# Optimization experiments

Measured on AMD Instinct MI355X. Metric: run time of the kernel, lower is better.

Reference implementation:

```python
import jax, jax.numpy as jnp
import numpy as np

B, H, W, D, C = 4, 16, 16, 16, 32

def setup_inputs() -> dict:
    key = jax.random.key(0)
    ks = jax.random.split(key, 13)
    s = 0.05
    return {
        "inputs": jax.random.normal(ks[0], (B, H, W, D, C), jnp.float32),
        "beta": jax.random.normal(ks[1], (1,), jnp.float32) * s,
        "wq": jax.random.normal(ks[2], (C, C), jnp.float32) * s,
        "bq": jax.random.normal(ks[3], (C,), jnp.float32) * s,
        "wk": jax.random.normal(ks[4], (C, C), jnp.float32) * s,
        "bk": jax.random.normal(ks[5], (C,), jnp.float32) * s,
        "wv": jax.random.normal(ks[6], (C, C), jnp.float32) * s,
        "bv": jax.random.normal(ks[7], (C,), jnp.float32) * s,
        "gamma": jax.random.normal(ks[8], (1,), jnp.float32) * s,
        "w_ch": jax.random.normal(ks[9], (1, 1, 4, C, C), jnp.float32) * s,
        "b_ch": jax.random.normal(ks[10], (C,), jnp.float32) * s,
        "w_pos": jax.random.normal(ks[11], (1, 1, 4, C, C), jnp.float32) * s,
        "b_pos": jax.random.normal(ks[12], (C,), jnp.float32) * s,
    }

def _conv3d_relu(x, w, b):
    # Conv3D kernel (1,1,4), VALID padding, then ReLU (activation='relu').
    y = jax.lax.conv_general_dilated(
        x, w, window_strides=(1, 1, 1), padding="VALID",
        dimension_numbers=("NDHWC", "DHWIO", "NDHWC"))
    return jax.nn.relu(y + b)

def reference(inputs, beta, wq, bq, wk, bk, wv, bv, gamma, w_ch, b_ch, w_pos, b_pos):
    b_, h, w, d, c = inputs.shape
    n = h * w * d  # flattened spatial-spectral volume

    # ---- Channel_attention (actually NxN spatial self-attention) ----
    q = inputs.reshape(b_, n, c)                       # (B,N,C)
    energy = jnp.einsum("bnc,bmc->bnm", q, q)          # (B,N,N) Q @ Q^T
    attn = jax.nn.softmax(energy, axis=-1)
    ca = jnp.einsum("bnm,bmc->bnc", attn, q)           # (B,N,C)
    ca = beta * ca.reshape(b_, h, w, d, c) + inputs

    # ---- Position_attention (CxC channel self-attention via 1x1x1 convs) ----
    Q = (jnp.einsum("bhwdc,cf->bhwdf", inputs, wq) + bq).reshape(b_, n, c)
    K = (jnp.einsum("bhwdc,cf->bhwdf", inputs, wk) + bk).reshape(b_, n, c)
    V = (jnp.einsum("bhwdc,cf->bhwdf", inputs, wv) + bv).reshape(b_, n, c)
    energy2 = jnp.einsum("bnc,bnf->bcf", Q, K)         # (B,C,C) = Q^T K
    attn2 = jax.nn.softmax(energy2, axis=-1)
    # out[b,n,f] = sum_c V[b,n,c] * attn2[b,f,c]  (V @ attn2^T per batch)
    pa = jnp.einsum("bnc,bfc->bnf", V, attn2)          # (B,N,C)
    pa = gamma * pa.reshape(b_, h, w, d, c) + inputs

    # ---- Attention_Embedding: conv3d(1,1,4)+relu on each branch, add ----
    # Dropout is identity at inference (training=False).
    out = _conv3d_relu(ca, w_ch, b_ch) + _conv3d_relu(pa, w_pos, b_pos)
    return out
```

## Files before the change

### kernel.cpp

```cpp
#include <hip/hip_runtime.h>
#include <cstddef>


typedef float f32x4 __attribute__((ext_vector_type(4)));
typedef short s16x8 __attribute__((ext_vector_type(8)));

#define SQRT_LOG2E 1.2011224087864498f
#define C2SHIFT    57.70780163555854f

__device__ inline unsigned cvtpk(float a, float b) {
  unsigned r;
  asm("v_cvt_pk_bf16_f32 %0, %1, %2" : "=v"(r) : "v"(a), "v"(b));
  return r;
}

__global__ __launch_bounds__(256) void k_prepgram(
    const float* __restrict__ x, ushort* __restrict__ xb, ushort* __restrict__ xtf,
    float* __restrict__ pG, float* __restrict__ pS)
{
  int bx = blockIdx.x, tid = threadIdx.x;
  if (bx < 256) {
    int t = bx * 256 + tid;
    const float4* xs = (const float4*)x;
    float4 v0 = xs[2 * t], v1 = xs[2 * t + 1];
    uint4 o;
    o.x = cvtpk(v0.x * SQRT_LOG2E, v0.y * SQRT_LOG2E);
    o.y = cvtpk(v0.z * SQRT_LOG2E, v0.w * SQRT_LOG2E);
    o.z = cvtpk(v1.x * SQRT_LOG2E, v1.y * SQRT_LOG2E);
    o.w = cvtpk(v1.z * SQRT_LOG2E, v1.w * SQRT_LOG2E);
    ((uint4*)xb)[t] = o;

    int b = t >> 14, r2 = t & 16383;
    int ktile = r2 >> 7, r3 = r2 & 127;
    int h = r3 >> 6, lane = r3 & 63;
    int g = lane >> 4, c = h * 16 + (lane & 15);
    const float* src = x + (((size_t)b * 4096 + ktile * 32 + 8 * g) * 32 + c);
    float w[8];
#pragma unroll
    for (int j = 0; j < 8; ++j) w[j] = src[(size_t)j * 32];
    uint4 u;
    u.x = cvtpk(w[0], w[1]); u.y = cvtpk(w[2], w[3]);
    u.z = cvtpk(w[4], w[5]); u.w = cvtpk(w[6], w[7]);
    ((uint4*)xtf)[(size_t)((b * 128 + ktile) * 2 + h) * 64 + lane] = u;
    return;
  }

  int gb = bx - 256;
  int b = gb >> 3, ks = gb & 7;
  int wid = tid >> 6, lane = tid & 63;
  int g = lane >> 4, c16 = lane & 15;
  f32x4 z = {0.f, 0.f, 0.f, 0.f};
  f32x4 G00 = z, G01 = z, G10 = z, G11 = z, s0 = z, s1 = z;
  s16x8 ones;
#pragma unroll
  for (int j = 0; j < 8; ++j) ones[j] = (short)0x3F80;
  int t0 = ks * 16 + wid * 4;
  for (int t = t0; t < t0 + 4; ++t) {
    s16x8 fr0, fr1;
    {
      const float* src = x + (((size_t)b * 4096 + t * 32 + 8 * g) * 32 + c16);
      float w[8];
#pragma unroll
      for (int j = 0; j < 8; ++j) w[j] = src[(size_t)j * 32];
      uint4 u2 = make_uint4(cvtpk(w[0], w[1]), cvtpk(w[2], w[3]),
                            cvtpk(w[4], w[5]), cvtpk(w[6], w[7]));
      fr0 = __builtin_bit_cast(s16x8, u2);
    }
    {
      const float* src = x + (((size_t)b * 4096 + t * 32 + 8 * g) * 32 + 16 + c16);
      float w[8];
#pragma unroll
      for (int j = 0; j < 8; ++j) w[j] = src[(size_t)j * 32];
      uint4 u2 = make_uint4(cvtpk(w[0], w[1]), cvtpk(w[2], w[3]),
                            cvtpk(w[4], w[5]), cvtpk(w[6], w[7]));
      fr1 = __builtin_bit_cast(s16x8, u2);
    }
    G00 = __builtin_amdgcn_mfma_f32_16x16x32_bf16(fr0, fr0, G00, 0, 0, 0);
    G01 = __builtin_amdgcn_mfma_f32_16x16x32_bf16(fr0, fr1, G01, 0, 0, 0);
    G10 = __builtin_amdgcn_mfma_f32_16x16x32_bf16(fr1, fr0, G10, 0, 0, 0);
    G11 = __builtin_amdgcn_mfma_f32_16x16x32_bf16(fr1, fr1, G11, 0, 0, 0);
    s0  = __builtin_amdgcn_mfma_f32_16x16x32_bf16(fr0, ones, s0, 0, 0, 0);
    s1  = __builtin_amdgcn_mfma_f32_16x16x32_bf16(fr1, ones, s1, 0, 0, 0);
  }
  int p = gb * 4 + wid;
  float* pg = pG + (size_t)p * 1024;
#pragma unroll
  for (int hr = 0; hr < 2; ++hr)
#pragma unroll
    for (int hc = 0; hc < 2; ++hc) {
      f32x4 v = hr ? (hc ? G11 : G10) : (hc ? G01 : G00);
#pragma unroll
      for (int r = 0; r < 4; ++r)
        pg[(16 * hr + 4 * g + r) * 32 + 16 * hc + c16] = v[r];
    }
  if (c16 == 0) {
#pragma unroll
    for (int hr = 0; hr < 2; ++hr) {
      f32x4 v = hr ? s1 : s0;
#pragma unroll
      for (int r = 0; r < 4; ++r) pS[p * 32 + 16 * hr + 4 * g + r] = v[r];
    }
  }
}

__global__ __launch_bounds__(1024) void k_alg(
    const float* __restrict__ pG, const float* __restrict__ pS,
    const float* __restrict__ wq, const float* __restrict__ bq,
    const float* __restrict__ wk, const float* __restrict__ bk,
    const float* __restrict__ wv, const float* __restrict__ bv,
    const float* __restrict__ gamma,
    const float* __restrict__ wpos, const float* __restrict__ bpos,
    float* __restrict__ w2, float* __restrict__ b2)
{
  __shared__ float G[1024], s[32], t1[1024], att[1024], M[1024], mvec[32];
  __shared__ float wqS[1024], wkS[1024], wvS[1024], wpoS[4096];
  int b = blockIdx.x, tid = threadIdx.x;
  if (tid < 256)      ((float4*)wqS)[tid] = ((const float4*)wq)[tid];
  else if (tid < 512) ((float4*)wkS)[tid - 256] = ((const float4*)wk)[tid - 256];
  else if (tid < 768) ((float4*)wvS)[tid - 512] = ((const float4*)wv)[tid - 512];
  ((float4*)wpoS)[tid] = ((const float4*)wpos)[tid];

  {
    const float* pg = pG + (size_t)b * 32 * 1024 + tid;
    float g0 = 0.f;
#pragma unroll
    for (int j = 0; j < 32; ++j) g0 += pg[(size_t)j * 1024];
    G[tid] = g0;
  }
  if (tid < 32) {
    const float* ps = pS + b * 32 * 32 + tid;
    float sv = 0.f;
#pragma unroll
    for (int j = 0; j < 32; ++j) sv += ps[j * 32];
    s[tid] = sv;
  }
  __syncthreads();

  int c = tid >> 5, f = tid & 31;
  float t = 0.f;
#pragma unroll
  for (int j = 0; j < 32; ++j) t = fmaf(G[c * 32 + j], wkS[j * 32 + f], t);
  t1[tid] = t;
  __syncthreads();
  float swk = 0.f, swq = 0.f;
#pragma unroll
  for (int j = 0; j < 32; ++j) {
    swk = fmaf(s[j], wkS[j * 32 + f], swk);
    swq = fmaf(s[j], wqS[j * 32 + c], swq);
  }
  float e = 0.f;
#pragma unroll
  for (int i = 0; i < 32; ++i) e = fmaf(wqS[i * 32 + c], t1[i * 32 + f], e);
  e += bq[c] * (swk + 4096.f * bk[f]) + swq * bk[f];
  float m_ = e;
  for (int off = 16; off; off >>= 1) m_ = fmaxf(m_, __shfl_xor(m_, off, 32));
  float pr = __expf(e - m_);
  float sum = pr;
  for (int off = 16; off; off >>= 1) sum += __shfl_xor(sum, off, 32);
  att[tid] = pr / sum;
  __syncthreads();
  float mm = 0.f;
#pragma unroll
  for (int j = 0; j < 32; ++j) mm = fmaf(wvS[c * 32 + j], att[f * 32 + j], mm);
  M[c * 32 + f] = mm;
  if (c == 0) {
    float mv = 0.f;
#pragma unroll
    for (int j = 0; j < 32; ++j) mv = fmaf(bv[j], att[f * 32 + j], mv);
    mvec[f] = mv;
  }
  __syncthreads();
  float gam = gamma[0];
  for (int kd = 0; kd < 4; ++kd) {
    float acc = 0.f;
#pragma unroll
    for (int j = 0; j < 32; ++j)
      acc = fmaf(M[c * 32 + j], wpoS[(kd * 32 + j) * 32 + f], acc);
    w2[((b * 4 + kd) * 32 + c) * 32 + f] = gam * acc + wpoS[(kd * 32 + c) * 32 + f];
  }
  if (c == 0) {
    float acc = 0.f;
#pragma unroll
    for (int kd = 0; kd < 4; ++kd)
#pragma unroll
      for (int j = 0; j < 32; ++j)
        acc = fmaf(mvec[j], wpoS[(kd * 32 + j) * 32 + tid], acc);
    b2[b * 32 + tid] = gam * acc + bpos[tid];
  }
}

union BigSh {
  char stage[4][2][8192];
  struct { f32x4 pO0[3][4][64]; f32x4 pO1[3][4][64]; float pL[3][4][64]; } ph1;
  struct { float4 wc[1024]; float4 wp[1024]; } ph2;
};

__global__ __launch_bounds__(1024) void k_fused(
    const ushort* __restrict__ xb, const ushort* __restrict__ xtf,
    const float* __restrict__ x, const float* __restrict__ beta,
    const float* __restrict__ wch, const float* __restrict__ bch,
    const float* __restrict__ w2, const float* __restrict__ b2,
    float* __restrict__ out)
{
  __shared__ BigSh u;
  __shared__ float sS[64][32];
  __shared__ float bcS[32], bpS[32];
  int rg = blockIdx.x, b = blockIdx.y, tid = threadIdx.x;
  if (tid < 32) { bcS[tid] = bch[tid]; bpS[tid] = b2[b * 32 + tid]; }

  int wid = tid >> 6, lane = tid & 63, g = lane >> 4, c16 = lane & 15;
  int wid2 = wid & 3, kh = wid >> 2;
  int qw = rg * 64 + wid2 * 16;
  const ushort* xbb = xb + ((size_t)b << 17);
  const ushort* xtb = xtf + (size_t)b * 131072;

  s16x8 qA = *(const s16x8*)(xbb + (qw + c16) * 32 + 8 * g);
  f32x4 z = {0.f, 0.f, 0.f, 0.f};
  f32x4 minit = {-C2SHIFT, -C2SHIFT, -C2SHIFT, -C2SHIFT};
  f32x4 oA0 = z, oA1 = z, lac = z;
  s16x8 ones;
#pragma unroll
  for (int j = 0; j < 8; ++j) ones[j] = (short)0x3F80;
  int kap = ((c16 >> 2) << 3) + (c16 & 3);
  int k0 = kh * 1024;

  int wtid = wid2 * 64 + lane;
  int srow = wtid >> 2, sslot = wtid & 3;
  int wslot = (sslot ^ (srow & 3)) << 4;
  int rslot = (g ^ (c16 & 3)) << 4;
  uint4 rkf, rxt;

#define LOADG(t) {                                                             \
    int kt = k0 + (t) * 64;                                                    \
    rkf = *(const uint4*)(xbb + (size_t)(kt + srow) * 32 + sslot * 8);         \
    rxt = *(const uint4*)(xtb + (size_t)(kt >> 5) * 1024 + wtid * 8);          \
  }
#define WRITES(bi) {                                                           \
    char* dst = u.stage[kh][bi];                                               \
    *(uint4*)(dst + srow * 64 + wslot) = rkf;                                  \
    *(uint4*)(dst + 4096 + wtid * 16) = rxt;                                   \
  }

  LOADG(0)
  WRITES(0)
  __syncthreads();

  for (int t = 0; t < 16; ++t) {
    if (t < 15) LOADG(t + 1)
    {
      const char* buf = u.stage[kh][t & 1];
      s16x8 kf0a = *(const s16x8*)(buf + kap * 64 + rslot);
      s16x8 kf1a = *(const s16x8*)(buf + (kap + 4) * 64 + rslot);
      s16x8 kf0b = *(const s16x8*)(buf + (32 + kap) * 64 + rslot);
      s16x8 kf1b = *(const s16x8*)(buf + (36 + kap) * 64 + rslot);
      const char* xt = buf + 4096 + lane * 16;
      s16x8 a0a = *(const s16x8*)(xt);
      s16x8 a1a = *(const s16x8*)(xt + 1024);
      s16x8 a0b = *(const s16x8*)(xt + 2048);
      s16x8 a1b = *(const s16x8*)(xt + 3072);

      __builtin_amdgcn_s_setprio(1);
      f32x4 e0 = __builtin_amdgcn_mfma_f32_16x16x32_bf16(kf0a, qA, minit, 0, 0, 0);
      f32x4 e1 = __builtin_amdgcn_mfma_f32_16x16x32_bf16(kf1a, qA, minit, 0, 0, 0);
      f32x4 e2 = __builtin_amdgcn_mfma_f32_16x16x32_bf16(kf0b, qA, minit, 0, 0, 0);
      f32x4 e3 = __builtin_amdgcn_mfma_f32_16x16x32_bf16(kf1b, qA, minit, 0, 0, 0);
      __builtin_amdgcn_s_setprio(0);
      f32x4 p0, p1, p2, p3;
#pragma unroll
      for (int r = 0; r < 4; ++r) {
        p0[r] = __builtin_amdgcn_exp2f(e0[r]);
        p1[r] = __builtin_amdgcn_exp2f(e1[r]);
        p2[r] = __builtin_amdgcn_exp2f(e2[r]);
        p3[r] = __builtin_amdgcn_exp2f(e3[r]);
      }
      uint4 uA = make_uint4(cvtpk(p0[0], p0[1]), cvtpk(p0[2], p0[3]),
                            cvtpk(p1[0], p1[1]), cvtpk(p1[2], p1[3]));
      uint4 uB = make_uint4(cvtpk(p2[0], p2[1]), cvtpk(p2[2], p2[3]),
                            cvtpk(p3[0], p3[1]), cvtpk(p3[2], p3[3]));
      s16x8 fpa = __builtin_bit_cast(s16x8, uA);
      s16x8 fpb = __builtin_bit_cast(s16x8, uB);

      __builtin_amdgcn_s_setprio(1);
      oA0 = __builtin_amdgcn_mfma_f32_16x16x32_bf16(a0a, fpa, oA0, 0, 0, 0);
      oA1 = __builtin_amdgcn_mfma_f32_16x16x32_bf16(a1a, fpa, oA1, 0, 0, 0);
      lac = __builtin_amdgcn_mfma_f32_16x16x32_bf16(ones, fpa, lac, 0, 0, 0);
      oA0 = __builtin_amdgcn_mfma_f32_16x16x32_bf16(a0b, fpb, oA0, 0, 0, 0);
      oA1 = __builtin_amdgcn_mfma_f32_16x16x32_bf16(a1b, fpb, oA1, 0, 0, 0);
      lac = __builtin_amdgcn_mfma_f32_16x16x32_bf16(ones, fpb, lac, 0, 0, 0);
      __builtin_amdgcn_s_setprio(0);
    }
    if (t < 15) WRITES((t + 1) & 1)
    __syncthreads();
  }
#undef LOADG
#undef WRITES

  if (kh != 0) {
    u.ph1.pO0[kh - 1][wid2][lane] = oA0;
    u.ph1.pO1[kh - 1][wid2][lane] = oA1;
    u.ph1.pL[kh - 1][wid2][lane] = lac[0];
  }
  __syncthreads();
  if (kh == 0) {
    float L = lac[0];
    f32x4 t0 = oA0, t1 = oA1;
#pragma unroll
    for (int q = 0; q < 3; ++q) {
      f32x4 q0 = u.ph1.pO0[q][wid2][lane], q1 = u.ph1.pO1[q][wid2][lane];
      L += u.ph1.pL[q][wid2][lane];
#pragma unroll
      for (int r = 0; r < 4; ++r) { t0[r] += q0[r]; t1[r] += q1[r]; }
    }
    float sc = beta[0] / L;
    int rloc = wid2 * 16 + c16;
    f32x4 v0, v1;
#pragma unroll
    for (int r = 0; r < 4; ++r) { v0[r] = t0[r] * sc; v1[r] = t1[r] * sc; }
    *(f32x4*)&sS[rloc][4 * g] = v0;
    *(f32x4*)&sS[rloc][16 + 4 * g] = v1;
  }
  __syncthreads();
  u.ph2.wc[tid] = ((const float4*)wch)[tid];
  u.ph2.wp[tid] = ((const float4*)(w2 + (size_t)b * 4096))[tid];
  __syncthreads();

  if (tid < 416) {
    int row2 = tid >> 3, fq = tid & 7;
    int hw_l = row2 / 13, dout = row2 % 13;
    int rbase = hw_l * 16 + dout;
    size_t xrow = ((size_t)b * 4096 + (size_t)(rg * 4 + hw_l) * 16 + dout) * 32;
    float accC[4], accP[4];
#pragma unroll
    for (int j = 0; j < 4; ++j) { accC[j] = bcS[fq * 4 + j]; accP[j] = bpS[fq * 4 + j]; }
    for (int kd = 0; kd < 4; ++kd) {
      const float4* xr4 = (const float4*)(x + xrow + (size_t)kd * 32);
      const float* srow2 = sS[rbase + kd];
#pragma unroll
      for (int c4 = 0; c4 < 8; ++c4) {
        float4 xv = xr4[c4];
#pragma unroll
        for (int e = 0; e < 4; ++e) {
          float xve = (e == 0 ? xv.x : e == 1 ? xv.y : e == 2 ? xv.z : xv.w);
          float cve = srow2[4 * c4 + e] + xve;
          int wbase = (kd * 32 + 4 * c4 + e) * 8 + fq;
          float4 w1 = u.ph2.wc[wbase];
          accC[0] = fmaf(cve, w1.x, accC[0]);
          accC[1] = fmaf(cve, w1.y, accC[1]);
          accC[2] = fmaf(cve, w1.z, accC[2]);
          accC[3] = fmaf(cve, w1.w, accC[3]);
          float4 w2v = u.ph2.wp[wbase];
          accP[0] = fmaf(xve, w2v.x, accP[0]);
          accP[1] = fmaf(xve, w2v.y, accP[1]);
          accP[2] = fmaf(xve, w2v.z, accP[2]);
          accP[3] = fmaf(xve, w2v.w, accP[3]);
        }
      }
    }
    int gid = b * 3328 + (rg * 4 + hw_l) * 13 + dout;
    float* orow = out + (size_t)gid * 32 + fq * 4;
    float4 o;
    o.x = fmaxf(accC[0], 0.f) + fmaxf(accP[0], 0.f);
    o.y = fmaxf(accC[1], 0.f) + fmaxf(accP[1], 0.f);
    o.z = fmaxf(accC[2], 0.f) + fmaxf(accP[2], 0.f);
    o.w = fmaxf(accC[3], 0.f) + fmaxf(accP[3], 0.f);
    *(float4*)orow = o;
  }
}

extern "C" void kernel_launch(void* const* d_in, const int* in_sizes, int n_in,
                              void* d_out, int out_size, void* d_ws, size_t ws_size,
                              hipStream_t stream)
{
  const float* x     = (const float*)d_in[0];
  const float* beta  = (const float*)d_in[1];
  const float* wq    = (const float*)d_in[2];
  const float* bq    = (const float*)d_in[3];
  const float* wk    = (const float*)d_in[4];
  const float* bk    = (const float*)d_in[5];
  const float* wv    = (const float*)d_in[6];
  const float* bv    = (const float*)d_in[7];
  const float* gamma = (const float*)d_in[8];
  const float* wch   = (const float*)d_in[9];
  const float* bch   = (const float*)d_in[10];
  const float* wpos  = (const float*)d_in[11];
  const float* bpos  = (const float*)d_in[12];
  float* out = (float*)d_out;
  float* ws  = (float*)d_ws;

  ushort* xb  = (ushort*)(ws + 0);
  ushort* xtf = (ushort*)(ws + 262144);
  float*  w2  = ws + 524288;
  float*  b2  = ws + 540672;
  float*  pG  = ws + 540800;
  float*  pS  = ws + 671872;

  hipLaunchKernelGGL(k_prepgram, dim3(288),   dim3(256),  0, stream,
                     x, xb, xtf, pG, pS);
  hipLaunchKernelGGL(k_alg,      dim3(4),     dim3(1024), 0, stream,
                     pG, pS, wq, bq, wk, bk, wv, bv, gamma, wpos, bpos, w2, b2);
  hipLaunchKernelGGL(k_fused,    dim3(64, 4), dim3(1024), 0, stream,
                     xb, xtf, x, beta, wch, bch, w2, b2, out);
}
```

Before: 42.72 us.

## Fuse per-batch channel-attention algebra kernel into main fused kernel

```diff
diff --git a/kernel.cpp b/kernel.cpp
--- a/kernel.cpp
+++ b/kernel.cpp
@@ -103,110 +103,31 @@
   }
 }
 
-__global__ __launch_bounds__(1024) void k_alg(
+union BigSh {
+  char stage[4][2][8192];
+  struct { f32x4 pO0[3][4][64]; f32x4 pO1[3][4][64]; float pL[3][4][64]; } ph1;
+  struct { float4 wc[1024]; float4 wp[1024]; } ph2;
+};
+
+__global__ __launch_bounds__(1024) void k_fused(
+    const ushort* __restrict__ xb, const ushort* __restrict__ xtf,
+    const float* __restrict__ x, const float* __restrict__ beta,
     const float* __restrict__ pG, const float* __restrict__ pS,
     const float* __restrict__ wq, const float* __restrict__ bq,
     const float* __restrict__ wk, const float* __restrict__ bk,
     const float* __restrict__ wv, const float* __restrict__ bv,
     const float* __restrict__ gamma,
+    const float* __restrict__ wch, const float* __restrict__ bch,
     const float* __restrict__ wpos, const float* __restrict__ bpos,
-    float* __restrict__ w2, float* __restrict__ b2)
-{
-  __shared__ float G[1024], s[32], t1[1024], att[1024], M[1024], mvec[32];
-  __shared__ float wqS[1024], wkS[1024], wvS[1024], wpoS[4096];
-  int b = blockIdx.x, tid = threadIdx.x;
-  if (tid < 256)      ((float4*)wqS)[tid] = ((const float4*)wq)[tid];
-  else if (tid < 512) ((float4*)wkS)[tid - 256] = ((const float4*)wk)[tid - 256];
-  else if (tid < 768) ((float4*)wvS)[tid - 512] = ((const float4*)wv)[tid - 512];
-  ((float4*)wpoS)[tid] = ((const float4*)wpos)[tid];
-
-  {
-    const float* pg = pG + (size_t)b * 32 * 1024 + tid;
-    float g0 = 0.f;
-#pragma unroll
-    for (int j = 0; j < 32; ++j) g0 += pg[(size_t)j * 1024];
-    G[tid] = g0;
-  }
-  if (tid < 32) {
-    const float* ps = pS + b * 32 * 32 + tid;
-    float sv = 0.f;
-#pragma unroll
-    for (int j = 0; j < 32; ++j) sv += ps[j * 32];
-    s[tid] = sv;
-  }
-  __syncthreads();
-
-  int c = tid >> 5, f = tid & 31;
-  float t = 0.f;
-#pragma unroll
-  for (int j = 0; j < 32; ++j) t = fmaf(G[c * 32 + j], wkS[j * 32 + f], t);
-  t1[tid] = t;
-  __syncthreads();
-  float swk = 0.f, swq = 0.f;
-#pragma unroll
-  for (int j = 0; j < 32; ++j) {
-    swk = fmaf(s[j], wkS[j * 32 + f], swk);
-    swq = fmaf(s[j], wqS[j * 32 + c], swq);
-  }
-  float e = 0.f;
-#pragma unroll
-  for (int i = 0; i < 32; ++i) e = fmaf(wqS[i * 32 + c], t1[i * 32 + f], e);
-  e += bq[c] * (swk + 4096.f * bk[f]) + swq * bk[f];
-  float m_ = e;
-  for (int off = 16; off; off >>= 1) m_ = fmaxf(m_, __shfl_xor(m_, off, 32));
-  float pr = __expf(e - m_);
-  float sum = pr;
-  for (int off = 16; off; off >>= 1) sum += __shfl_xor(sum, off, 32);
-  att[tid] = pr / sum;
-  __syncthreads();
-  float mm = 0.f;
-#pragma unroll
-  for (int j = 0; j < 32; ++j) mm = fmaf(wvS[c * 32 + j], att[f * 32 + j], mm);
-  M[c * 32 + f] = mm;
-  if (c == 0) {
-    float mv = 0.f;
-#pragma unroll
-    for (int j = 0; j < 32; ++j) mv = fmaf(bv[j], att[f * 32 + j], mv);
-    mvec[f] = mv;
-  }
-  __syncthreads();
-  float gam = gamma[0];
-  for (int kd = 0; kd < 4; ++kd) {
-    float acc = 0.f;
-#pragma unroll
-    for (int j = 0; j < 32; ++j)
-      acc = fmaf(M[c * 32 + j], wpoS[(kd * 32 + j) * 32 + f], acc);
-    w2[((b * 4 + kd) * 32 + c) * 32 + f] = gam * acc + wpoS[(kd * 32 + c) * 32 + f];
-  }
-  if (c == 0) {
-    float acc = 0.f;
-#pragma unroll
-    for (int kd = 0; kd < 4; ++kd)
-#pragma unroll
-      for (int j = 0; j < 32; ++j)
-        acc = fmaf(mvec[j], wpoS[(kd * 32 + j) * 32 + tid], acc);
-    b2[b * 32 + tid] = gam * acc + bpos[tid];
-  }
-}
-
-union BigSh {
-  char stage[4][2][8192];
-  struct { f32x4 pO0[3][4][64]; f32x4 pO1[3][4][64]; float pL[3][4][64]; } ph1;
-  struct { float4 wc[1024]; float4 wp[1024]; } ph2;
-};
-
-__global__ __launch_bounds__(1024) void k_fused(
-    const ushort* __restrict__ xb, const ushort* __restrict__ xtf,
-    const float* __restrict__ x, const float* __restrict__ beta,
-    const float* __restrict__ wch, const float* __restrict__ bch,
-    const float* __restrict__ w2, const float* __restrict__ b2,
     float* __restrict__ out)
 {
   __shared__ BigSh u;
   __shared__ float sS[64][32];
   __shared__ float bcS[32], bpS[32];
+  __shared__ float aG[1024], as_[32], at1[1024], aatt[1024], aM[1024], amv[32];
+  __shared__ float awq[1024], awk[1024], awv[1024], awpo[4096];
   int rg = blockIdx.x, b = blockIdx.y, tid = threadIdx.x;
-  if (tid < 32) { bcS[tid] = bch[tid]; bpS[tid] = b2[b * 32 + tid]; }
+  if (tid < 32) bcS[tid] = bch[tid];
 
   int wid = tid >> 6, lane = tid & 63, g = lane >> 4, c16 = lane & 15;
   int wid2 = wid & 3, kh = wid >> 2;
@@ -319,9 +240,81 @@
     *(f32x4*)&sS[rloc][4 * g] = v0;
     *(f32x4*)&sS[rloc][16 + 4 * g] = v1;
   }
+  if (tid < 256)      ((float4*)awq)[tid] = ((const float4*)wq)[tid];
+  else if (tid < 512) ((float4*)awk)[tid - 256] = ((const float4*)wk)[tid - 256];
+  else if (tid < 768) ((float4*)awv)[tid - 512] = ((const float4*)wv)[tid - 512];
+  ((float4*)awpo)[tid] = ((const float4*)wpos)[tid];
+  {
+    const float* pg = pG + (size_t)b * 32 * 1024 + tid;
+    float g0 = 0.f;
+#pragma unroll
+    for (int j = 0; j < 32; ++j) g0 += pg[(size_t)j * 1024];
+    aG[tid] = g0;
+  }
+  if (tid < 32) {
+    const float* ps = pS + b * 32 * 32 + tid;
+    float sv = 0.f;
+#pragma unroll
+    for (int j = 0; j < 32; ++j) sv += ps[j * 32];
+    as_[tid] = sv;
+  }
   __syncthreads();
+
+  {
+    int c = tid >> 5, f = tid & 31;
+    float t = 0.f;
+#pragma unroll
+    for (int j = 0; j < 32; ++j) t = fmaf(aG[c * 32 + j], awk[j * 32 + f], t);
+    at1[tid] = t;
+    __syncthreads();
+    float swk = 0.f, swq = 0.f;
+#pragma unroll
+    for (int j = 0; j < 32; ++j) {
+      swk = fmaf(as_[j], awk[j * 32 + f], swk);
+      swq = fmaf(as_[j], awq[j * 32 + c], swq);
+    }
+    float e = 0.f;
+#pragma unroll
+    for (int i = 0; i < 32; ++i) e = fmaf(awq[i * 32 + c], at1[i * 32 + f], e);
+    e += bq[c] * (swk + 4096.f * bk[f]) + swq * bk[f];
+    float m_ = e;
+    for (int off = 16; off; off >>= 1) m_ = fmaxf(m_, __shfl_xor(m_, off, 32));
+    float pr = __expf(e - m_);
+    float sum = pr;
+    for (int off = 16; off; off >>= 1) sum += __shfl_xor(sum, off, 32);
+    aatt[tid] = pr / sum;
+    __syncthreads();
+    float mm = 0.f;
+#pragma unroll
+    for (int j = 0; j < 32; ++j) mm = fmaf(awv[c * 32 + j], aatt[f * 32 + j], mm);
+    aM[c * 32 + f] = mm;
+    if (c == 0) {
+      float mv = 0.f;
+#pragma unroll
+      for (int j = 0; j < 32; ++j) mv = fmaf(bv[j], aatt[f * 32 + j], mv);
+      amv[f] = mv;
+    }
+    __syncthreads();
+    float gam = gamma[0];
+    float* wpf = (float*)u.ph2.wp;
+    for (int kd = 0; kd < 4; ++kd) {
+      float acc = 0.f;
+#pragma unroll
+      for (int j = 0; j < 32; ++j)
+        acc = fmaf(aM[c * 32 + j], awpo[(kd * 32 + j) * 32 + f], acc);
+      wpf[(kd * 32 + c) * 32 + f] = gam * acc + awpo[(kd * 32 + c) * 32 + f];
+    }
+    if (c == 0) {
+      float acc = 0.f;
+#pragma unroll
+      for (int kd = 0; kd < 4; ++kd)
+#pragma unroll
+        for (int j = 0; j < 32; ++j)
+          acc = fmaf(amv[j], awpo[(kd * 32 + j) * 32 + tid], acc);
+      bpS[tid] = gam * acc + bpos[tid];
+    }
+  }
   u.ph2.wc[tid] = ((const float4*)wch)[tid];
-  u.ph2.wp[tid] = ((const float4*)(w2 + (size_t)b * 4096))[tid];
   __syncthreads();
 
   if (tid < 416) {
@@ -389,15 +382,12 @@
 
   ushort* xb  = (ushort*)(ws + 0);
   ushort* xtf = (ushort*)(ws + 262144);
-  float*  w2  = ws + 524288;
-  float*  b2  = ws + 540672;
-  float*  pG  = ws + 540800;
-  float*  pS  = ws + 671872;
+  float*  pG  = ws + 524288;
+  float*  pS  = ws + 655360;
 
   hipLaunchKernelGGL(k_prepgram, dim3(288),   dim3(256),  0, stream,
                      x, xb, xtf, pG, pS);
-  hipLaunchKernelGGL(k_alg,      dim3(4),     dim3(1024), 0, stream,
-                     pG, pS, wq, bq, wk, bk, wv, bv, gamma, wpos, bpos, w2, b2);
   hipLaunchKernelGGL(k_fused,    dim3(64, 4), dim3(1024), 0, stream,
-                     xb, xtf, x, beta, wch, bch, w2, b2, out);
+                     xb, xtf, x, beta, pG, pS,
+                     wq, bq, wk, bk, wv, bv, gamma, wch, bch, wpos, bpos, out);
 }
```

Result: slower. 46.30 us (+8.4%).
